# Kernel optimization log

Measured on AMD Instinct MI355X. Metric: run time of the kernel, lower is better.

Reference implementation:

```python
import jax, jax.numpy as jnp
import numpy as np

N_NODES = 100000
N_EDGES = 1600000
HIDDEN = 128
OUT_DIM = 1
N_GRAPHS = 2048
VOCAB = 28  # atom types, Embedding(28, hidden_dim)


def setup_inputs() -> dict:
    key = jax.random.key(0)
    ks = jax.random.split(key, 14)
    s = 1.0 / np.sqrt(HIDDEN)
    inp = {
        "x_idx": jax.random.randint(ks[0], (N_NODES,), 0, VOCAB, dtype=jnp.int32),
        "edge_src": jax.random.randint(ks[1], (N_EDGES,), 0, N_NODES, dtype=jnp.int32),
        "edge_dst": jax.random.randint(ks[2], (N_EDGES,), 0, N_NODES, dtype=jnp.int32),
        "batch": jnp.sort(jax.random.randint(ks[3], (N_NODES,), 0, N_GRAPHS, dtype=jnp.int32)),
        # parameters
        "embed": jax.random.normal(ks[4], (VOCAB, HIDDEN), dtype=jnp.float32) * 0.02,
        "eps0": jnp.zeros((1,), dtype=jnp.float32),
        "w1_0": jax.random.normal(ks[5], (HIDDEN, HIDDEN), dtype=jnp.float32) * s,
        "b1_0": jnp.zeros((HIDDEN,), dtype=jnp.float32),
        "w2_0": jax.random.normal(ks[6], (HIDDEN, HIDDEN), dtype=jnp.float32) * s,
        "b2_0": jnp.zeros((HIDDEN,), dtype=jnp.float32),
        "eps1": jnp.zeros((1,), dtype=jnp.float32),
        "w1_1": jax.random.normal(ks[7], (HIDDEN, HIDDEN), dtype=jnp.float32) * s,
        "b1_1": jnp.zeros((HIDDEN,), dtype=jnp.float32),
        "w2_1": jax.random.normal(ks[8], (HIDDEN, OUT_DIM), dtype=jnp.float32) * s,
        "b2_1": jnp.zeros((OUT_DIM,), dtype=jnp.float32),
    }
    return inp


def _gin_layer(x, edge_src, edge_dst, eps, w1, b1, w2, b2):
    # A @ x via edge-list SpMM: out[dst] += x[src]  (same math as to_dense().matmul(x))
    agg = jax.ops.segment_sum(x[edge_src], edge_dst, num_segments=N_NODES)
    h = agg + (1.0 + eps) * x  # [N, in_feats]; eps broadcasts (shape [1])
    h = h @ w1 + b1            # linear1 (no nonlinearity between, as in source)
    return h @ w2 + b2         # linear2


def reference(x_idx, edge_src, edge_dst, batch, embed,
              eps0, w1_0, b1_0, w2_0, b2_0,
              eps1, w1_1, b1_1, w2_1, b2_1):
    x = embed[x_idx]  # [N, HIDDEN] — Embedding lookup (.squeeze(1) trivial here)
    x = jax.nn.relu(_gin_layer(x, edge_src, edge_dst, eps0, w1_0, b1_0, w2_0, b2_0))
    x = _gin_layer(x, edge_src, edge_dst, eps1, w1_1, b1_1, w2_1, b2_1)  # [N, 1]
    y_hat = jax.ops.segment_sum(x.squeeze(-1), batch, num_segments=N_GRAPHS)  # [G]
    return (y_hat, x)
```

## Files before the change

kernel.cpp:

```cpp
#include <hip/hip_runtime.h>

#define N_NODES  100000
#define N_EDGES  1600000
#define HIDDEN   128
#define N_GRAPHS 2048
#define VOCAB    28
#define NB       256
#define NPB      392
#define CAP      7000
#define NBIN     512
#define EPB      3125
#define EPT      4
#define CSTR     29
#define MAGIC    2804876602ULL

__global__ __launch_bounds__(256) void k_init(float* __restrict__ out,
                                              int* __restrict__ gcursor) {
    int i = blockIdx.x * 256 + threadIdx.x;
    if (i < N_GRAPHS) out[i] = 0.0f;
    else if (i < N_GRAPHS + NB) gcursor[i - N_GRAPHS] = 0;
}

__global__ __launch_bounds__(1024) void k_binprep(const int* __restrict__ esrc,
                                                  const int* __restrict__ edst,
                                                  const int* __restrict__ x_idx,
                                                  unsigned* __restrict__ binned,
                                                  int* __restrict__ gcursor,
                                                  const float* __restrict__ embed,
                                                  const float* __restrict__ w1_0,
                                                  const float* __restrict__ w2_0,
                                                  const float* __restrict__ b1_0,
                                                  const float* __restrict__ b2_0,
                                                  const float* __restrict__ w1_1,
                                                  const float* __restrict__ b1_1,
                                                  const float* __restrict__ w2_1,
                                                  const float* __restrict__ b2_1,
                                                  float* __restrict__ T,
                                                  float* __restrict__ bc0,
                                                  float* __restrict__ wc1,
                                                  float* __restrict__ bc1) {
    const int tid = threadIdx.x;
    const int bid = blockIdx.x;

    if (bid >= NBIN) {
        if (bid < NBIN + 4) {
            int g = (bid - NBIN) * 1024 + tid;
            if (g < VOCAB * HIDDEN) {
                int i = g >> 7, j = g & 127;
                float s = 0.f;
#pragma unroll 8
                for (int k = 0; k < HIDDEN; ++k)
                    s += embed[i * HIDDEN + k] * w1_0[k * HIDDEN + j];
                T[g] = s;
            }
        } else {
            if (tid < 128) {
                float s = 0.f;
#pragma unroll 8
                for (int k = 0; k < HIDDEN; ++k)
                    s += b1_0[k] * w2_0[k * HIDDEN + tid];
                bc0[tid] = s + b2_0[tid];
                if (tid == 0) {
                    float q = 0.f;
                    for (int k = 0; k < HIDDEN; ++k) q += b1_1[k] * w2_1[k];
                    bc1[0] = q + b2_1[0];
                }
            } else if (tid < 256) {
                int i = tid - 128;
                float s = 0.f;
#pragma unroll 8
                for (int k = 0; k < HIDDEN; ++k)
                    s += w1_1[i * HIDDEN + k] * w2_1[k];
                wc1[i] = s;
            }
        }
        return;
    }

    __shared__ int hist[NB];
    __shared__ int lcur[NB];
    __shared__ int gbase[NB];

    if (tid < NB) { hist[tid] = 0; lcur[tid] = 0; }
    __syncthreads();

    unsigned mypk[EPT];
    short    myb[EPT];
#pragma unroll
    for (int i = 0; i < EPT; ++i) {
        int idx = i * 1024 + tid;
        myb[i] = -1;
        if (idx < EPB) {
            int e   = bid * EPB + idx;
            int dst = edst[e];
            int src = esrc[e];
            int b   = (int)(((unsigned long long)dst * MAGIC) >> 40);
            int dl  = dst - b * NPB;
            int vix = x_idx[src];
            mypk[i] = ((unsigned)dl << 22) | ((unsigned)vix << 17) | (unsigned)src;
            myb[i]  = (short)b;
            atomicAdd(&hist[b], 1);
        }
    }
    __syncthreads();

    if (tid < NB) {
        int v = hist[tid];
        gbase[tid] = (v > 0) ? atomicAdd(&gcursor[tid], v) : 0;
    }
    __syncthreads();

#pragma unroll
    for (int i = 0; i < EPT; ++i) {
        if (myb[i] >= 0) {
            int b  = myb[i];
            int lr = atomicAdd(&lcur[b], 1);
            binned[(size_t)b * CAP + gbase[b] + lr] = mypk[i];
        }
    }
}

__global__ __launch_bounds__(1024) void k_prep2(const float* __restrict__ T,
                                                const float* __restrict__ w2_0,
                                                float* __restrict__ EW) {
    int g = blockIdx.x * 1024 + threadIdx.x;
    if (g >= VOCAB * HIDDEN) return;
    int i = g >> 7, j = g & 127;
    float s = 0.f;
#pragma unroll 8
    for (int k = 0; k < HIDDEN; ++k)
        s += T[i * HIDDEN + k] * w2_0[k * HIDDEN + j];
    EW[g] = s;
}

__global__ __launch_bounds__(1024) void k_layerC(const unsigned* __restrict__ binned,
                                                 const int* __restrict__ gcursor,
                                                 const int* __restrict__ x_idx,
                                                 const float* __restrict__ EW,
                                                 const float* __restrict__ bc0,
                                                 const float* __restrict__ wc1,
                                                 const float* __restrict__ eps0,
                                                 float* __restrict__ d) {
    __shared__ int lcnt[NPB * CSTR];

    const int tid = threadIdx.x;
    const int b   = blockIdx.x;

    for (int i = tid; i < NPB * CSTR; i += 1024) lcnt[i] = 0;
    __syncthreads();

    const int cnt = gcursor[b];
    const unsigned* bp = binned + (size_t)b * CAP;
    for (int i = tid; i < cnt; i += 1024) {
        unsigned pk = bp[i];
        atomicAdd(&lcnt[(pk >> 22) * CSTR + ((pk >> 17) & 31)], 1);
    }
    __syncthreads();

    if (tid >= NPB) return;

    const int n      = b * NPB + tid;
    const bool valid = (n < N_NODES);
    const int xi     = valid ? x_idx[n] : 0;
    const float s    = 1.0f + eps0[0];

    float cf[VOCAB];
#pragma unroll
    for (int v = 0; v < VOCAB; ++v)
        cf[v] = (float)lcnt[tid * CSTR + v] + ((v == xi) ? s : 0.0f);

    const float4* EW4 = reinterpret_cast<const float4*>(EW);
    const float4* b04 = reinterpret_cast<const float4*>(bc0);
    const float4* w14 = reinterpret_cast<const float4*>(wc1);

    float dacc = 0.f;
#pragma unroll 1
    for (int f4 = 0; f4 < 32; ++f4) {
        float4 a = b04[f4];
#pragma unroll
        for (int v = 0; v < VOCAB; ++v) {
            float4 e = EW4[v * 32 + f4];
            a.x += cf[v] * e.x;
            a.y += cf[v] * e.y;
            a.z += cf[v] * e.z;
            a.w += cf[v] * e.w;
        }
        float4 w = w14[f4];
        dacc += fmaxf(a.x, 0.f) * w.x + fmaxf(a.y, 0.f) * w.y
              + fmaxf(a.z, 0.f) * w.z + fmaxf(a.w, 0.f) * w.w;
    }
    if (valid) d[n] = dacc;
}

__global__ __launch_bounds__(1024) void k_B2(const unsigned* __restrict__ binned,
                                             const int* __restrict__ gcursor,
                                             const float* __restrict__ d,
                                             const int* __restrict__ batch,
                                             const float* __restrict__ eps1,
                                             const float* __restrict__ bc1,
                                             float* __restrict__ out) {
    __shared__ float racc[NPB];
    __shared__ float gacc[N_GRAPHS];

    const int tid = threadIdx.x;
    const int b   = blockIdx.x;
    const int n0  = b * NPB;
    const int nlast = min(n0 + NPB - 1, N_NODES - 1);

    if (tid < NPB) racc[tid] = 0.f;
    const int g0 = batch[n0];
    const int g1 = batch[nlast];
    for (int g = g0 + tid; g <= g1; g += 1024) gacc[g] = 0.f;
    __syncthreads();

    const int cnt = gcursor[b];
    const unsigned* bp = binned + (size_t)b * CAP;
    for (int i = tid; i < cnt; i += 1024) {
        unsigned pk = bp[i];
        atomicAdd(&racc[pk >> 22], d[pk & 0x1FFFFu]);
    }
    __syncthreads();

    int n = n0 + tid;
    if (tid < NPB && n < N_NODES) {
        float r = (1.0f + eps1[0]) * d[n] + racc[tid] + bc1[0];
        out[N_GRAPHS + n] = r;
        atomicAdd(&gacc[batch[n]], r);
    }
    __syncthreads();
    for (int g = g0 + tid; g <= g1; g += 1024) {
        float v = gacc[g];
        if (v != 0.f) atomicAdd(&out[g], v);
    }
}

extern "C" void kernel_launch(void* const* d_in, const int* in_sizes, int n_in,
                              void* d_out, int out_size, void* d_ws, size_t ws_size,
                              hipStream_t stream) {
    const int*   x_idx = (const int*)d_in[0];
    const int*   esrc  = (const int*)d_in[1];
    const int*   edst  = (const int*)d_in[2];
    const int*   batch = (const int*)d_in[3];
    const float* embed = (const float*)d_in[4];
    const float* eps0  = (const float*)d_in[5];
    const float* w1_0  = (const float*)d_in[6];
    const float* b1_0  = (const float*)d_in[7];
    const float* w2_0  = (const float*)d_in[8];
    const float* b2_0  = (const float*)d_in[9];
    const float* eps1  = (const float*)d_in[10];
    const float* w1_1  = (const float*)d_in[11];
    const float* b1_1  = (const float*)d_in[12];
    const float* w2_1  = (const float*)d_in[13];
    const float* b2_1  = (const float*)d_in[14];

    float* out = (float*)d_out;

    int*      gcursor = (int*)d_ws;
    unsigned* binned  = (unsigned*)(gcursor + 512);
    float*    d       = (float*)(binned + (size_t)NB * CAP);
    float*    T       = d + 100352;
    float*    bc0     = T + VOCAB * HIDDEN;
    float*    wc1     = bc0 + HIDDEN;
    float*    bc1     = wc1 + HIDDEN;
    float*    EW      = bc1 + 1;

    k_init<<<9, 256, 0, stream>>>(out, gcursor);

    k_binprep<<<NBIN + 5, 1024, 0, stream>>>(esrc, edst, x_idx, binned, gcursor,
                                             embed, w1_0, w2_0, b1_0, b2_0,
                                             w1_1, b1_1, w2_1, b2_1,
                                             T, bc0, wc1, bc1);

    k_prep2<<<4, 1024, 0, stream>>>(T, w2_0, EW);

    k_layerC<<<NB, 1024, 0, stream>>>(binned, gcursor, x_idx, EW, bc0, wc1, eps0, d);

    k_B2<<<NB, 1024, 0, stream>>>(binned, gcursor, d, batch, eps1, bc1, out);
}
```

Baseline: 164.8 us.

## Fuse all stages into one cooperative kernel with grid-wide syncs

Replaces the five separate launches (init, binning/prep, prep2, layer C, B2) with a single cooperative kernel of 256 blocks that uses grid.sync between phases. Each block now bins twice as many edges, and block 0 also computes both weight-folding matmuls, keeping the intermediate in shared memory. The aim is to remove launch overhead and inter-kernel gaps. In exchange, binning runs on only 256 blocks instead of 512, block 0 carries the serial weight-prep work before the second barrier, and grid syncs add their own cost.

```diff
diff --git a/kernel.cpp b/kernel.cpp
--- a/kernel.cpp
+++ b/kernel.cpp
@@ -1,4 +1,7 @@
 #include <hip/hip_runtime.h>
+#include <hip/hip_cooperative_groups.h>
+
+namespace cg = cooperative_groups;
 
 #define N_NODES  100000
 #define N_EDGES  1600000
@@ -8,52 +11,96 @@
 #define NB       256
 #define NPB      392
 #define CAP      7000
-#define NBIN     512
-#define EPB      3125
-#define EPT      4
+#define EPB      6250
+#define EPT      7
 #define CSTR     29
 #define MAGIC    2804876602ULL
 
-__global__ __launch_bounds__(256) void k_init(float* __restrict__ out,
-                                              int* __restrict__ gcursor) {
-    int i = blockIdx.x * 256 + threadIdx.x;
-    if (i < N_GRAPHS) out[i] = 0.0f;
-    else if (i < N_GRAPHS + NB) gcursor[i - N_GRAPHS] = 0;
-}
-
-__global__ __launch_bounds__(1024) void k_binprep(const int* __restrict__ esrc,
-                                                  const int* __restrict__ edst,
-                                                  const int* __restrict__ x_idx,
-                                                  unsigned* __restrict__ binned,
-                                                  int* __restrict__ gcursor,
-                                                  const float* __restrict__ embed,
-                                                  const float* __restrict__ w1_0,
-                                                  const float* __restrict__ w2_0,
-                                                  const float* __restrict__ b1_0,
-                                                  const float* __restrict__ b2_0,
-                                                  const float* __restrict__ w1_1,
-                                                  const float* __restrict__ b1_1,
-                                                  const float* __restrict__ w2_1,
-                                                  const float* __restrict__ b2_1,
-                                                  float* __restrict__ T,
-                                                  float* __restrict__ bc0,
-                                                  float* __restrict__ wc1,
-                                                  float* __restrict__ bc1) {
+__global__ __launch_bounds__(1024) void k_fused(
+    const int* __restrict__ esrc, const int* __restrict__ edst,
+    const int* __restrict__ x_idx, const int* __restrict__ batch,
+    const float* __restrict__ embed, const float* __restrict__ eps0,
+    const float* __restrict__ w1_0, const float* __restrict__ b1_0,
+    const float* __restrict__ w2_0, const float* __restrict__ b2_0,
+    const float* __restrict__ eps1,
+    const float* __restrict__ w1_1, const float* __restrict__ b1_1,
+    const float* __restrict__ w2_1, const float* __restrict__ b2_1,
+    unsigned* __restrict__ binned, int* __restrict__ gcursor,
+    float* __restrict__ dvec, float* __restrict__ EW,
+    float* __restrict__ bc0, float* __restrict__ wc1,
+    float* __restrict__ bc1, float* __restrict__ out)
+{
+    cg::grid_group grid = cg::this_grid();
+    __shared__ int smem[NPB * CSTR];
+
     const int tid = threadIdx.x;
     const int bid = blockIdx.x;
 
-    if (bid >= NBIN) {
-        if (bid < NBIN + 4) {
-            int g = (bid - NBIN) * 1024 + tid;
-            if (g < VOCAB * HIDDEN) {
+    if (tid == 0) gcursor[bid] = 0;
+    if (bid < 2) out[bid * 1024 + tid] = 0.f;
+    grid.sync();
+
+    {
+        int* hist  = smem;
+        int* lcur  = smem + 256;
+        int* gbase = smem + 512;
+        if (tid < NB) { hist[tid] = 0; lcur[tid] = 0; }
+        __syncthreads();
+
+        unsigned mypk[EPT];
+        short    myb[EPT];
+#pragma unroll
+        for (int i = 0; i < EPT; ++i) {
+            int idx = i * 1024 + tid;
+            myb[i] = -1;
+            if (idx < EPB) {
+                int e   = bid * EPB + idx;
+                int dst = edst[e];
+                int src = esrc[e];
+                int b   = (int)(((unsigned long long)dst * MAGIC) >> 40);
+                int dl  = dst - b * NPB;
+                int vix = x_idx[src];
+                mypk[i] = ((unsigned)dl << 22) | ((unsigned)vix << 17) | (unsigned)src;
+                myb[i]  = (short)b;
+                atomicAdd(&hist[b], 1);
+            }
+        }
+        __syncthreads();
+
+        if (tid < NB) {
+            int v = hist[tid];
+            gbase[tid] = (v > 0) ? atomicAdd(&gcursor[tid], v) : 0;
+        }
+        __syncthreads();
+
+#pragma unroll
+        for (int i = 0; i < EPT; ++i) {
+            if (myb[i] >= 0) {
+                int b  = myb[i];
+                int lr = atomicAdd(&lcur[b], 1);
+                binned[(size_t)b * CAP + gbase[b] + lr] = mypk[i];
+            }
+        }
+
+        if (bid == 0) {
+            float* Tl = reinterpret_cast<float*>(smem + 1024);
+            for (int g = tid; g < VOCAB * HIDDEN; g += 1024) {
                 int i = g >> 7, j = g & 127;
                 float s = 0.f;
 #pragma unroll 8
                 for (int k = 0; k < HIDDEN; ++k)
                     s += embed[i * HIDDEN + k] * w1_0[k * HIDDEN + j];
-                T[g] = s;
-            }
-        } else {
+                Tl[g] = s;
+            }
+            __syncthreads();
+            for (int g = tid; g < VOCAB * HIDDEN; g += 1024) {
+                int i = g >> 7, j = g & 127;
+                float s = 0.f;
+#pragma unroll 8
+                for (int k = 0; k < HIDDEN; ++k)
+                    s += Tl[i * HIDDEN + k] * w2_0[k * HIDDEN + j];
+                EW[g] = s;
+            }
             if (tid < 128) {
                 float s = 0.f;
 #pragma unroll 8
@@ -74,163 +121,89 @@
                 wc1[i] = s;
             }
         }
-        return;
     }
-
-    __shared__ int hist[NB];
-    __shared__ int lcur[NB];
-    __shared__ int gbase[NB];
-
-    if (tid < NB) { hist[tid] = 0; lcur[tid] = 0; }
-    __syncthreads();
-
-    unsigned mypk[EPT];
-    short    myb[EPT];
-#pragma unroll
-    for (int i = 0; i < EPT; ++i) {
-        int idx = i * 1024 + tid;
-        myb[i] = -1;
-        if (idx < EPB) {
-            int e   = bid * EPB + idx;
-            int dst = edst[e];
-            int src = esrc[e];
-            int b   = (int)(((unsigned long long)dst * MAGIC) >> 40);
-            int dl  = dst - b * NPB;
-            int vix = x_idx[src];
-            mypk[i] = ((unsigned)dl << 22) | ((unsigned)vix << 17) | (unsigned)src;
-            myb[i]  = (short)b;
-            atomicAdd(&hist[b], 1);
+    grid.sync();
+
+    {
+        int* lcnt = smem;
+        for (int i = tid; i < NPB * CSTR; i += 1024) lcnt[i] = 0;
+        __syncthreads();
+
+        const int cnt = gcursor[bid];
+        const unsigned* bp = binned + (size_t)bid * CAP;
+        for (int i = tid; i < cnt; i += 1024) {
+            unsigned pk = bp[i];
+            atomicAdd(&lcnt[(pk >> 22) * CSTR + ((pk >> 17) & 31)], 1);
+        }
+        __syncthreads();
+
+        if (tid < NPB) {
+            const int n      = bid * NPB + tid;
+            const bool valid = (n < N_NODES);
+            const int xi     = valid ? x_idx[n] : 0;
+            const float s    = 1.0f + eps0[0];
+
+            float cf[VOCAB];
+#pragma unroll
+            for (int v = 0; v < VOCAB; ++v)
+                cf[v] = (float)lcnt[tid * CSTR + v] + ((v == xi) ? s : 0.0f);
+
+            const float4* EW4 = reinterpret_cast<const float4*>(EW);
+            const float4* b04 = reinterpret_cast<const float4*>(bc0);
+            const float4* w14 = reinterpret_cast<const float4*>(wc1);
+
+            float dacc = 0.f;
+#pragma unroll 1
+            for (int f4 = 0; f4 < 32; ++f4) {
+                float4 a = b04[f4];
+#pragma unroll
+                for (int v = 0; v < VOCAB; ++v) {
+                    float4 e = EW4[v * 32 + f4];
+                    a.x += cf[v] * e.x;
+                    a.y += cf[v] * e.y;
+                    a.z += cf[v] * e.z;
+                    a.w += cf[v] * e.w;
+                }
+                float4 w = w14[f4];
+                dacc += fmaxf(a.x, 0.f) * w.x + fmaxf(a.y, 0.f) * w.y
+                      + fmaxf(a.z, 0.f) * w.z + fmaxf(a.w, 0.f) * w.w;
+            }
+            if (valid) dvec[n] = dacc;
         }
     }
-    __syncthreads();
-
-    if (tid < NB) {
-        int v = hist[tid];
-        gbase[tid] = (v > 0) ? atomicAdd(&gcursor[tid], v) : 0;
-    }
-    __syncthreads();
-
-#pragma unroll
-    for (int i = 0; i < EPT; ++i) {
-        if (myb[i] >= 0) {
-            int b  = myb[i];
-            int lr = atomicAdd(&lcur[b], 1);
-            binned[(size_t)b * CAP + gbase[b] + lr] = mypk[i];
-        }
-    }
-}
-
-__global__ __launch_bounds__(1024) void k_prep2(const float* __restrict__ T,
-                                                const float* __restrict__ w2_0,
-                                                float* __restrict__ EW) {
-    int g = blockIdx.x * 1024 + threadIdx.x;
-    if (g >= VOCAB * HIDDEN) return;
-    int i = g >> 7, j = g & 127;
-    float s = 0.f;
-#pragma unroll 8
-    for (int k = 0; k < HIDDEN; ++k)
-        s += T[i * HIDDEN + k] * w2_0[k * HIDDEN + j];
-    EW[g] = s;
-}
-
-__global__ __launch_bounds__(1024) void k_layerC(const unsigned* __restrict__ binned,
-                                                 const int* __restrict__ gcursor,
-                                                 const int* __restrict__ x_idx,
-                                                 const float* __restrict__ EW,
-                                                 const float* __restrict__ bc0,
-                                                 const float* __restrict__ wc1,
-                                                 const float* __restrict__ eps0,
-                                                 float* __restrict__ d) {
-    __shared__ int lcnt[NPB * CSTR];
-
-    const int tid = threadIdx.x;
-    const int b   = blockIdx.x;
-
-    for (int i = tid; i < NPB * CSTR; i += 1024) lcnt[i] = 0;
-    __syncthreads();
-
-    const int cnt = gcursor[b];
-    const unsigned* bp = binned + (size_t)b * CAP;
-    for (int i = tid; i < cnt; i += 1024) {
-        unsigned pk = bp[i];
-        atomicAdd(&lcnt[(pk >> 22) * CSTR + ((pk >> 17) & 31)], 1);
-    }
-    __syncthreads();
-
-    if (tid >= NPB) return;
-
-    const int n      = b * NPB + tid;
-    const bool valid = (n < N_NODES);
-    const int xi     = valid ? x_idx[n] : 0;
-    const float s    = 1.0f + eps0[0];
-
-    float cf[VOCAB];
-#pragma unroll
-    for (int v = 0; v < VOCAB; ++v)
-        cf[v] = (float)lcnt[tid * CSTR + v] + ((v == xi) ? s : 0.0f);
-
-    const float4* EW4 = reinterpret_cast<const float4*>(EW);
-    const float4* b04 = reinterpret_cast<const float4*>(bc0);
-    const float4* w14 = reinterpret_cast<const float4*>(wc1);
-
-    float dacc = 0.f;
-#pragma unroll 1
-    for (int f4 = 0; f4 < 32; ++f4) {
-        float4 a = b04[f4];
-#pragma unroll
-        for (int v = 0; v < VOCAB; ++v) {
-            float4 e = EW4[v * 32 + f4];
-            a.x += cf[v] * e.x;
-            a.y += cf[v] * e.y;
-            a.z += cf[v] * e.z;
-            a.w += cf[v] * e.w;
-        }
-        float4 w = w14[f4];
-        dacc += fmaxf(a.x, 0.f) * w.x + fmaxf(a.y, 0.f) * w.y
-              + fmaxf(a.z, 0.f) * w.z + fmaxf(a.w, 0.f) * w.w;
-    }
-    if (valid) d[n] = dacc;
-}
-
-__global__ __launch_bounds__(1024) void k_B2(const unsigned* __restrict__ binned,
-                                             const int* __restrict__ gcursor,
-                                             const float* __restrict__ d,
-                                             const int* __restrict__ batch,
-                                             const float* __restrict__ eps1,
-                                             const float* __restrict__ bc1,
-                                             float* __restrict__ out) {
-    __shared__ float racc[NPB];
-    __shared__ float gacc[N_GRAPHS];
-
-    const int tid = threadIdx.x;
-    const int b   = blockIdx.x;
-    const int n0  = b * NPB;
-    const int nlast = min(n0 + NPB - 1, N_NODES - 1);
-
-    if (tid < NPB) racc[tid] = 0.f;
-    const int g0 = batch[n0];
-    const int g1 = batch[nlast];
-    for (int g = g0 + tid; g <= g1; g += 1024) gacc[g] = 0.f;
-    __syncthreads();
-
-    const int cnt = gcursor[b];
-    const unsigned* bp = binned + (size_t)b * CAP;
-    for (int i = tid; i < cnt; i += 1024) {
-        unsigned pk = bp[i];
-        atomicAdd(&racc[pk >> 22], d[pk & 0x1FFFFu]);
-    }
-    __syncthreads();
-
-    int n = n0 + tid;
-    if (tid < NPB && n < N_NODES) {
-        float r = (1.0f + eps1[0]) * d[n] + racc[tid] + bc1[0];
-        out[N_GRAPHS + n] = r;
-        atomicAdd(&gacc[batch[n]], r);
-    }
-    __syncthreads();
-    for (int g = g0 + tid; g <= g1; g += 1024) {
-        float v = gacc[g];
-        if (v != 0.f) atomicAdd(&out[g], v);
+    grid.sync();
+
+    {
+        float* racc = reinterpret_cast<float*>(smem);
+        float* gacc = reinterpret_cast<float*>(smem + 512);
+        const int n0    = bid * NPB;
+        const int nlast = min(n0 + NPB - 1, N_NODES - 1);
+
+        if (tid < NPB) racc[tid] = 0.f;
+        const int g0 = batch[n0];
+        const int g1 = batch[nlast];
+        for (int g = g0 + tid; g <= g1; g += 1024) gacc[g] = 0.f;
+        __syncthreads();
+
+        const int cnt = gcursor[bid];
+        const unsigned* bp = binned + (size_t)bid * CAP;
+        for (int i = tid; i < cnt; i += 1024) {
+            unsigned pk = bp[i];
+            atomicAdd(&racc[pk >> 22], dvec[pk & 0x1FFFFu]);
+        }
+        __syncthreads();
+
+        int n = n0 + tid;
+        if (tid < NPB && n < N_NODES) {
+            float r = (1.0f + eps1[0]) * dvec[n] + racc[tid] + bc1[0];
+            out[N_GRAPHS + n] = r;
+            atomicAdd(&gacc[batch[n]], r);
+        }
+        __syncthreads();
+        for (int g = g0 + tid; g <= g1; g += 1024) {
+            float v = gacc[g];
+            if (v != 0.f) atomicAdd(&out[g], v);
+        }
     }
 }
 
@@ -257,23 +230,21 @@
 
     int*      gcursor = (int*)d_ws;
     unsigned* binned  = (unsigned*)(gcursor + 512);
-    float*    d       = (float*)(binned + (size_t)NB * CAP);
-    float*    T       = d + 100352;
-    float*    bc0     = T + VOCAB * HIDDEN;
+    float*    dvec    = (float*)(binned + (size_t)NB * CAP);
+    float*    EW      = dvec + 100352;
+    float*    bc0     = EW + VOCAB * HIDDEN;
     float*    wc1     = bc0 + HIDDEN;
     float*    bc1     = wc1 + HIDDEN;
-    float*    EW      = bc1 + 1;
-
-    k_init<<<9, 256, 0, stream>>>(out, gcursor);
-
-    k_binprep<<<NBIN + 5, 1024, 0, stream>>>(esrc, edst, x_idx, binned, gcursor,
-                                             embed, w1_0, w2_0, b1_0, b2_0,
-                                             w1_1, b1_1, w2_1, b2_1,
-                                             T, bc0, wc1, bc1);
-
-    k_prep2<<<4, 1024, 0, stream>>>(T, w2_0, EW);
-
-    k_layerC<<<NB, 1024, 0, stream>>>(binned, gcursor, x_idx, EW, bc0, wc1, eps0, d);
-
-    k_B2<<<NB, 1024, 0, stream>>>(binned, gcursor, d, batch, eps1, bc1, out);
+
+    void* args[] = {
+        (void*)&esrc, (void*)&edst, (void*)&x_idx, (void*)&batch,
+        (void*)&embed, (void*)&eps0,
+        (void*)&w1_0, (void*)&b1_0, (void*)&w2_0, (void*)&b2_0,
+        (void*)&eps1, (void*)&w1_1, (void*)&b1_1, (void*)&w2_1, (void*)&b2_1,
+        (void*)&binned, (void*)&gcursor, (void*)&dvec, (void*)&EW,
+        (void*)&bc0, (void*)&wc1, (void*)&bc1, (void*)&out
+    };
+
+    hipLaunchCooperativeKernel((const void*)k_fused, dim3(NB), dim3(1024),
+                               args, 0, stream);
 }
```

Result: slower. 317.6 us (+92.7%).

## Double destination bins to 512 and fold prep GEMMs into init and bin kernels

Applied to the files above, without the earlier changes.

Destination nodes are now split into 512 bins of 196 nodes instead of 256 bins of 392, so the layer kernels launch 512 blocks with smaller per-bin work, which should improve occupancy across the CUs. The first weight-product GEMM moves into the init kernel and the second one moves into the binning kernel, which removes the separate k_prep2 launch. Smaller bins bring more global cursor atomics and a tighter per-bin capacity, which raises the risk of overflow if the edge distribution is skewed. The shared-memory count table is smaller, which may allow more resident blocks per CU.

```diff
diff --git a/kernel.cpp b/kernel.cpp
--- a/kernel.cpp
+++ b/kernel.cpp
@@ -5,40 +5,53 @@
 #define HIDDEN   128
 #define N_GRAPHS 2048
 #define VOCAB    28
-#define NB       256
-#define NPB      392
-#define CAP      7000
+#define NB       512
+#define NPB      196
+#define CAP      3600
 #define NBIN     512
 #define EPB      3125
 #define EPT      4
 #define CSTR     29
-#define MAGIC    2804876602ULL
+#define MAGIC196 1402438302ULL
 
 __global__ __launch_bounds__(256) void k_init(float* __restrict__ out,
-                                              int* __restrict__ gcursor) {
-    int i = blockIdx.x * 256 + threadIdx.x;
-    if (i < N_GRAPHS) out[i] = 0.0f;
-    else if (i < N_GRAPHS + NB) gcursor[i - N_GRAPHS] = 0;
-}
-
-__global__ __launch_bounds__(1024) void k_binprep(const int* __restrict__ esrc,
-                                                  const int* __restrict__ edst,
-                                                  const int* __restrict__ x_idx,
-                                                  unsigned* __restrict__ binned,
-                                                  int* __restrict__ gcursor,
-                                                  const float* __restrict__ embed,
-                                                  const float* __restrict__ w1_0,
-                                                  const float* __restrict__ w2_0,
-                                                  const float* __restrict__ b1_0,
-                                                  const float* __restrict__ b2_0,
-                                                  const float* __restrict__ w1_1,
-                                                  const float* __restrict__ b1_1,
-                                                  const float* __restrict__ w2_1,
-                                                  const float* __restrict__ b2_1,
-                                                  float* __restrict__ T,
-                                                  float* __restrict__ bc0,
-                                                  float* __restrict__ wc1,
-                                                  float* __restrict__ bc1) {
+                                              int* __restrict__ gcursor,
+                                              const float* __restrict__ embed,
+                                              const float* __restrict__ w1_0,
+                                              float* __restrict__ T) {
+    const int bid = blockIdx.x, tid = threadIdx.x;
+    if (bid < 10) {
+        int i = bid * 256 + tid;
+        if (i < N_GRAPHS) out[i] = 0.0f;
+        else if (i < N_GRAPHS + NB) gcursor[i - N_GRAPHS] = 0;
+    } else {
+        int g = (bid - 10) * 256 + tid;
+        int i = g >> 7, j = g & 127;
+        float s = 0.f;
+#pragma unroll 8
+        for (int k = 0; k < HIDDEN; ++k)
+            s += embed[i * HIDDEN + k] * w1_0[k * HIDDEN + j];
+        T[g] = s;
+    }
+}
+
+__global__ __launch_bounds__(1024) void k_bin(const int* __restrict__ esrc,
+                                              const int* __restrict__ edst,
+                                              const int* __restrict__ x_idx,
+                                              unsigned* __restrict__ binned,
+                                              int* __restrict__ gcursor,
+                                              const float* __restrict__ T,
+                                              const float* __restrict__ w2_0,
+                                              const float* __restrict__ b1_0,
+                                              const float* __restrict__ b2_0,
+                                              const float* __restrict__ w1_1,
+                                              const float* __restrict__ b1_1,
+                                              const float* __restrict__ w2_1,
+                                              const float* __restrict__ b2_1,
+                                              float* __restrict__ EW,
+                                              float* __restrict__ bc0,
+                                              float* __restrict__ wc1,
+                                              float* __restrict__ bc1) {
     const int tid = threadIdx.x;
     const int bid = blockIdx.x;
 
@@ -50,8 +63,8 @@
                 float s = 0.f;
 #pragma unroll 8
                 for (int k = 0; k < HIDDEN; ++k)
-                    s += embed[i * HIDDEN + k] * w1_0[k * HIDDEN + j];
-                T[g] = s;
+                    s += T[i * HIDDEN + k] * w2_0[k * HIDDEN + j];
+                EW[g] = s;
             }
         } else {
             if (tid < 128) {
@@ -94,7 +107,7 @@
             int e   = bid * EPB + idx;
             int dst = edst[e];
             int src = esrc[e];
-            int b   = (int)(((unsigned long long)dst * MAGIC) >> 40);
+            int b   = (int)(((unsigned long long)dst * MAGIC196) >> 38);
             int dl  = dst - b * NPB;
             int vix = x_idx[src];
             mypk[i] = ((unsigned)dl << 22) | ((unsigned)vix << 17) | (unsigned)src;
@@ -118,19 +131,6 @@
             binned[(size_t)b * CAP + gbase[b] + lr] = mypk[i];
         }
     }
-}
-
-__global__ __launch_bounds__(1024) void k_prep2(const float* __restrict__ T,
-                                                const float* __restrict__ w2_0,
-                                                float* __restrict__ EW) {
-    int g = blockIdx.x * 1024 + threadIdx.x;
-    if (g >= VOCAB * HIDDEN) return;
-    int i = g >> 7, j = g & 127;
-    float s = 0.f;
-#pragma unroll 8
-    for (int k = 0; k < HIDDEN; ++k)
-        s += T[i * HIDDEN + k] * w2_0[k * HIDDEN + j];
-    EW[g] = s;
 }
 
 __global__ __launch_bounds__(1024) void k_layerC(const unsigned* __restrict__ binned,
@@ -257,23 +257,21 @@
 
     int*      gcursor = (int*)d_ws;
     unsigned* binned  = (unsigned*)(gcursor + 512);
-    float*    d       = (float*)(binned + (size_t)NB * CAP);
-    float*    T       = d + 100352;
-    float*    bc0     = T + VOCAB * HIDDEN;
+    float*    dvec    = (float*)(binned + (size_t)NB * CAP);
+    float*    T       = dvec + 100352;
+    float*    EW      = T + VOCAB * HIDDEN;
+    float*    bc0     = EW + VOCAB * HIDDEN;
     float*    wc1     = bc0 + HIDDEN;
     float*    bc1     = wc1 + HIDDEN;
-    float*    EW      = bc1 + 1;
-
-    k_init<<<9, 256, 0, stream>>>(out, gcursor);
-
-    k_binprep<<<NBIN + 5, 1024, 0, stream>>>(esrc, edst, x_idx, binned, gcursor,
-                                             embed, w1_0, w2_0, b1_0, b2_0,
-                                             w1_1, b1_1, w2_1, b2_1,
-                                             T, bc0, wc1, bc1);
-
-    k_prep2<<<4, 1024, 0, stream>>>(T, w2_0, EW);
-
-    k_layerC<<<NB, 1024, 0, stream>>>(binned, gcursor, x_idx, EW, bc0, wc1, eps0, d);
-
-    k_B2<<<NB, 1024, 0, stream>>>(binned, gcursor, d, batch, eps1, bc1, out);
-}
+
+    k_init<<<24, 256, 0, stream>>>(out, gcursor, embed, w1_0, T);
+
+    k_bin<<<NBIN + 5, 1024, 0, stream>>>(esrc, edst, x_idx, binned, gcursor,
+                                         T, w2_0, b1_0, b2_0,
+                                         w1_1, b1_1, w2_1, b2_1,
+                                         EW, bc0, wc1, bc1);
+
+    k_layerC<<<NB, 1024, 0, stream>>>(binned, gcursor, x_idx, EW, bc0, wc1, eps0, dvec);
+
+    k_B2<<<NB, 1024, 0, stream>>>(binned, gcursor, dvec, batch, eps1, bc1, out);
+}
```

After: 158.9 us. 3.5% less time.
